# Kernel optimization log

Measured on AMD Instinct MI355X. Metric: run time of the kernel, lower is better.

The kernel has to match this reference:

```python
import jax, jax.numpy as jnp
import numpy as np

L, H, E, FF, MAXP, NKNOW = 4, 8, 512, 2048, 10, 1000
B, S = 4, 128
HD = E // H


def _layer_norm(x, g, b, eps=1e-5):
    m = x.mean(-1, keepdims=True)
    v = ((x - m) ** 2).mean(-1, keepdims=True)
    return (x - m) / jnp.sqrt(v + eps) * g + b


def setup_inputs() -> dict:
    key = jax.random.key(0)
    ks = jax.random.split(key, 16)
    x = jax.random.normal(ks[0], (B, S, E), jnp.float32)
    adj = jax.random.randint(ks[1], (B, S, S), 0, 2, jnp.int32)
    s_mask = jax.random.randint(ks[2], (B, S, S), 0, 2, jnp.int32)
    o_mask = jax.random.randint(ks[3], (B, S, S), 0, 2, jnp.int32)
    knowledge = jax.random.normal(ks[4], (NKNOW, E), jnp.float32)
    know_adj = jax.random.randint(ks[5], (B, S, S), 0, NKNOW, jnp.int64)
    pos_mask = jax.random.randint(ks[6], (S, S), 0, MAXP + 1, jnp.int32)
    # relative position embedding tables (padding_idx=0 -> row 0 zero)
    pe_k = jax.random.normal(ks[7], (MAXP + 1, HD), jnp.float32).at[0].set(0.0)
    pe_v = jax.random.normal(ks[8], (MAXP + 1, HD), jnp.float32).at[0].set(0.0)
    sc = 0.02
    # stacked per-layer parameters
    Wq = jax.random.normal(ks[9], (L, E, E), jnp.float32) * sc
    Wk = jax.random.normal(ks[10], (L, E, E), jnp.float32) * sc
    Wvs = jax.random.normal(ks[11], (L, E, E), jnp.float32) * sc
    Wvo = jax.random.normal(ks[12], (L, E, E), jnp.float32) * sc
    Wo = jax.random.normal(ks[13], (L, E, E), jnp.float32) * sc
    Wkn = jax.random.normal(ks[14], (L, E, E), jnp.float32) * sc
    kf = jax.random.split(ks[15], 4)
    w1 = jax.random.normal(kf[0], (L, FF, E), jnp.float32) * sc
    b1 = jnp.zeros((L, FF), jnp.float32)
    w2 = jax.random.normal(kf[1], (L, E, FF), jnp.float32) * sc
    b2 = jnp.zeros((L, E), jnp.float32)
    ln1_g = jnp.ones((L, E), jnp.float32)
    ln1_b = jnp.zeros((L, E), jnp.float32)
    ln2_g = jnp.ones((L, E), jnp.float32)
    ln2_b = jnp.zeros((L, E), jnp.float32)
    return dict(x=x, adj=adj, s_mask=s_mask, o_mask=o_mask, knowledge=knowledge,
                know_adj=know_adj, pos_mask=pos_mask, pe_k=pe_k, pe_v=pe_v,
                Wq=Wq, Wk=Wk, Wvs=Wvs, Wvo=Wvo, Wo=Wo, Wkn=Wkn,
                ln1_g=ln1_g, ln1_b=ln1_b, w1=w1, b1=b1, w2=w2, b2=b2,
                ln2_g=ln2_g, ln2_b=ln2_b)


def reference(x, adj, s_mask, o_mask, knowledge, know_adj, pos_mask, pe_k, pe_v,
              Wq, Wk, Wvs, Wvo, Wo, Wkn, ln1_g, ln1_b, w1, b1, w2, b2,
              ln2_g, ln2_b):
    bsz, slen, emb = x.shape
    hd = emb // H
    scaling = float(hd) ** (-0.5)
    # relative position embeddings, shared across batch/heads: [S,S,hd]
    pos = jnp.clip(pos_mask, 0, MAXP)
    rel_k = pe_k[pos]
    rel_v = pe_v[pos]
    adj_f = adj.astype(x.dtype)[:, None, :, :]          # [B,1,S,S]
    sm = s_mask.astype(x.dtype)[:, None, :, :, None]    # [B,1,S,S,1]
    om = o_mask.astype(x.dtype)[:, None, :, :, None]
    know_feat = knowledge[know_adj]                      # [B,S,S,E]

    def split_heads(t):  # [B,S,E] -> [B,H,S,hd]
        return t.reshape(bsz, slen, H, hd).transpose(0, 2, 1, 3)

    h = x
    for i in range(L):
        q = split_heads(h @ Wq[i].T)
        k = split_heads(h @ Wk[i].T)
        vs = split_heads(h @ Wvs[i].T)
        vo = split_heads(h @ Wvo[i].T)
        # knowledge projection -> [B,H,S,S,hd]
        know = (know_feat @ Wkn[i].T).reshape(bsz, slen, slen, H, hd).transpose(0, 3, 1, 2, 4)
        # multiplicative attention: q_i * (k_j + know_ij + rel_ij) summed over hd
        rel = (know + rel_k[None, None]) + k[:, :, None, :, :]
        scores = jnp.einsum('bhid,bhijd->bhij', q, rel) * scaling
        scores = scores - (1.0 - adj_f) * 1e30          # mask_logic
        attn = jax.nn.softmax(scores, axis=-1)           # [B,H,S,S]
        value = vs[:, :, None, :, :] * sm + vo[:, :, None, :, :] * om  # [B,H,S,S,hd]
        attn_sum = jnp.einsum('bhijd,bhij->bhid', value + rel_v[None, None], attn)
        out = attn_sum.transpose(0, 2, 1, 3).reshape(bsz, slen, emb) @ Wo[i].T
        h = _layer_norm(h + out, ln1_g[i], ln1_b[i])
        ff = jax.nn.relu(h @ w1[i].T + b1[i]) @ w2[i].T + b2[i]
        h = _layer_norm(h + ff, ln2_g[i], ln2_b[i])
    return h
```

## Files before the change

### kernel.cpp

```cpp
#include <hip/hip_runtime.h>

#define EE 512
#define SS 128
#define BB 4
#define NH 8
#define HD 64
#define FFD 2048
#define NL 4
#define LDQ 2048
#define KEXT 320
#define PSTR 136

typedef short bf16x8 __attribute__((ext_vector_type(8)));
typedef float f32x4 __attribute__((ext_vector_type(4)));

__device__ __forceinline__ ushort f2bf(float f) {
    uint u = __float_as_uint(f);
    return (ushort)((u + 0x7fffu + ((u >> 16) & 1u)) >> 16);
}
__device__ __forceinline__ float bflo(uint u) { return __uint_as_float(u << 16); }
__device__ __forceinline__ float bfhi(uint u) { return __uint_as_float(u & 0xffff0000u); }

__device__ __forceinline__ void gll16(const ushort* g, ushort* l) {
    __builtin_amdgcn_global_load_lds(
        (const __attribute__((address_space(1))) void*)g,
        (__attribute__((address_space(3))) void*)l, 16, 0, 0);
}

struct GemmJob {
    const ushort* A; const ushort* B;
    float* Cf; ushort* Cb; ushort* vext;
    const float* bias; const float* resid;
    int M, N, K, flags, nbx, base;
};

__global__ __launch_bounds__(256) void gemm_bf16(GemmJob j0, GemmJob j1, int njobs)
{
    __shared__ ushort As[4][2048];
    __shared__ ushort Bs[4][4096];
    GemmJob j = (njobs > 1 && (int)blockIdx.x >= j1.base) ? j1 : j0;
    const int bid = (int)blockIdx.x - j.base;
    const int by = bid / j.nbx, bx = bid % j.nbx;
    const int rowBase = by * 32, colBase = bx * 64;
    const int t = threadIdx.x, lane = t & 63, wid = t >> 6;
    const int wc = wid;
    const int Kd = j.K, Md = j.M, Nd = j.N;

    const ushort* Bg = j.B + (size_t)(colBase + lane) * Kd;
    int gr = rowBase + (lane & 31); if (gr >= Md) gr = Md - 1;
    const ushort* Ag = j.A + (size_t)gr * Kd + (2 * wid + (lane >> 5)) * 8;

    f32x4 acc[2];
#pragma unroll
    for (int m = 0; m < 2; ++m)
#pragma unroll
        for (int r = 0; r < 4; ++r) acc[m][r] = 0.f;

    auto STAGE = [&](int bf, int tt) {
        const int k0 = tt << 6;
        gll16(Bg + k0 + (2 * wid) * 8,     &Bs[bf][(2 * wid) * 512]);
        gll16(Bg + k0 + (2 * wid + 1) * 8, &Bs[bf][(2 * wid + 1) * 512]);
        gll16(Ag + k0,                     &As[bf][(2 * wid) * 256]);
    };
    auto COMPUTE = [&](int bf) {
#pragma unroll
        for (int kc = 0; kc < 2; ++kc) {
            const int c16 = kc * 4 + (lane >> 4);
            bf16x8 af[2], bfg;
#pragma unroll
            for (int m = 0; m < 2; ++m) {
                const int row = m * 16 + (lane & 15);
                af[m] = *(const bf16x8*)&As[bf][c16 * 256 + row * 8];
            }
            {
                const int rowb = wc * 16 + (lane & 15);
                bfg = *(const bf16x8*)&Bs[bf][c16 * 512 + rowb * 8];
            }
#pragma unroll
            for (int m = 0; m < 2; ++m)
                acc[m] = __builtin_amdgcn_mfma_f32_16x16x32_bf16(af[m], bfg, acc[m], 0, 0, 0);
        }
    };

    const int nt = Kd >> 6;
    STAGE(0, 0); STAGE(1, 1); STAGE(2, 2);
    asm volatile("s_waitcnt vmcnt(6)" ::: "memory");
    __builtin_amdgcn_s_barrier();
    for (int tt = 0; tt < nt; ++tt) {
        if (tt + 3 < nt) STAGE((tt + 3) & 3, tt + 3);
        COMPUTE(tt & 3);
        if (tt < nt - 1) {
            if (tt + 3 < nt)      asm volatile("s_waitcnt vmcnt(6)" ::: "memory");
            else if (tt + 2 < nt) asm volatile("s_waitcnt vmcnt(3)" ::: "memory");
            else                  asm volatile("s_waitcnt vmcnt(0)" ::: "memory");
            __builtin_amdgcn_s_barrier();
        }
    }

    const int cl = lane & 15, rh = lane >> 4;
#pragma unroll
    for (int m = 0; m < 2; ++m) {
        const int col = colBase + wc * 16 + cl;
#pragma unroll
        for (int r = 0; r < 4; ++r) {
            const int rr = rowBase + m * 16 + rh * 4 + r;
            if (rr < Md) {
                float v = acc[m][r];
                if (j.flags & 1) v += j.bias[col];
                if (j.flags & 2) v = fmaxf(v, 0.f);
                if (j.resid) v += j.resid[(size_t)rr * Nd + col];
                if ((j.flags & 4) && col >= 1024) {
                    const int cc = col - 1024;
                    const int hh = (cc >> 6) & 7, d = cc & 63, vv = cc >> 9;
                    const int bb = rr >> 7, jj2 = rr & 127;
                    j.vext[((size_t)((bb * 8 + hh) * 64 + d)) * KEXT + vv * 128 + jj2] = f2bf(v);
                } else {
                    if (j.Cf) j.Cf[(size_t)rr * Nd + col] = v;
                    if (j.Cb) j.Cb[(size_t)rr * Nd + col] = f2bf(v);
                }
            }
        }
    }
}

__global__ __launch_bounds__(256) void score_gemm(
    const ushort* __restrict__ qkvv, const ushort* __restrict__ kprojl,
    float* __restrict__ qk, float* __restrict__ qkk)
{
    __shared__ ushort As[2048];
    __shared__ ushort Bs[4096];
    const int t = threadIdx.x, lane = t & 63, wid = t >> 6;
    const int bid = blockIdx.x;
    const ushort *Abase, *Bbase;
    float* Cbase; int crs, rowBase, colBase;
    if (bid < 256) {
        const int q = bid >> 3, sub = bid & 7;
        const int b = q >> 3, h = q & 7;
        rowBase = (sub >> 1) * 32; colBase = (sub & 1) * 64;
        Abase = qkvv + (size_t)(b * SS) * LDQ + h * HD;
        Bbase = qkvv + (size_t)(b * SS) * LDQ + 512 + h * HD;
        Cbase = qk + (size_t)b * 131072 + h * 128;
        crs = 1024;
    } else {
        const int idx = bid - 256;
        const int h = idx >> 8, sub = idx & 255;
        rowBase = (sub >> 4) * 32; colBase = (sub & 15) * 64;
        Abase = qkvv + h * HD;
        Bbase = kprojl + h * HD;
        Cbase = qkk + (size_t)h * 1024;
        crs = 8192;
    }
    {
        const ushort* Bg = Bbase + (size_t)(colBase + lane) * LDQ;
        const ushort* Ag = Abase + (size_t)(rowBase + (lane & 31)) * LDQ
                           + (2 * wid + (lane >> 5)) * 8;
        gll16(Bg + (2 * wid) * 8,     &Bs[(2 * wid) * 512]);
        gll16(Bg + (2 * wid + 1) * 8, &Bs[(2 * wid + 1) * 512]);
        gll16(Ag,                     &As[(2 * wid) * 256]);
        asm volatile("s_waitcnt vmcnt(0)" ::: "memory");
        __builtin_amdgcn_s_barrier();
    }
    f32x4 acc[2];
#pragma unroll
    for (int m = 0; m < 2; ++m)
#pragma unroll
        for (int r = 0; r < 4; ++r) acc[m][r] = 0.f;
#pragma unroll
    for (int kc = 0; kc < 2; ++kc) {
        const int c16 = kc * 4 + (lane >> 4);
        bf16x8 af[2], bfg;
#pragma unroll
        for (int m = 0; m < 2; ++m) {
            const int row = m * 16 + (lane & 15);
            af[m] = *(const bf16x8*)&As[c16 * 256 + row * 8];
        }
        {
            const int rowb = wid * 16 + (lane & 15);
            bfg = *(const bf16x8*)&Bs[c16 * 512 + rowb * 8];
        }
#pragma unroll
        for (int m = 0; m < 2; ++m)
            acc[m] = __builtin_amdgcn_mfma_f32_16x16x32_bf16(af[m], bfg, acc[m], 0, 0, 0);
    }
    const int cl = lane & 15, rh = lane >> 4;
#pragma unroll
    for (int m = 0; m < 2; ++m) {
        const int col = colBase + wid * 16 + cl;
        const int row0 = rowBase + m * 16 + rh * 4;
#pragma unroll
        for (int r = 0; r < 4; ++r)
            Cbase[(size_t)(row0 + r) * crs + col] = acc[m][r];
    }
}

__global__ __launch_bounds__(256) void pv_kernel(
    const ushort* __restrict__ vext, const float* __restrict__ qk,
    const float* __restrict__ qkk,
    const int* __restrict__ know_adj, const int* __restrict__ pos_mask,
    const int* __restrict__ adj, const int* __restrict__ s_mask,
    const int* __restrict__ o_mask, ushort* __restrict__ asum)
{
    __shared__ ushort Ps[40 * PSTR];
    __shared__ ushort Bs[40 * 512];
    __shared__ float ap[16][11];
    const int blk = blockIdx.x;
    const int ib = blk & 7, h = (blk >> 3) & 7, b = blk >> 6;
    const int t = threadIdx.x, lane = t & 63, wid = t >> 6;

    if (t < 176) ap[t / 11][t % 11] = 0.f;
    __syncthreads();

    {
        const ushort* vbase = vext + ((size_t)((b * 8 + h) * 64) + lane) * KEXT;
#pragma unroll
        for (int s = 0; s < 5; ++s) {
            const int c = s * 8 + wid * 2;
            gll16(vbase + c * 8,       &Bs[c * 512]);
            gll16(vbase + (c + 1) * 8, &Bs[(c + 1) * 512]);
        }
    }

    {
        const int r = t >> 4, g = t & 15;
        const int i = ib * 16 + r;
        const int tok = b * 128 + i;
        const float* qkrow  = qk + (size_t)b * 131072 + (size_t)i * 1024 + h * 128 + g * 8;
        const float* qkkrow = qkk + (size_t)tok * 8192 + h * 1024;
        const int base = tok * 128 + g * 8;
        const int pb   = i * 128 + g * 8;
        int4 kn0 = *(const int4*)(know_adj + base), kn1 = *(const int4*)(know_adj + base + 4);
        int4 ad0 = *(const int4*)(adj + base),      ad1 = *(const int4*)(adj + base + 4);
        int4 sm0 = *(const int4*)(s_mask + base),   sm1 = *(const int4*)(s_mask + base + 4);
        int4 om0 = *(const int4*)(o_mask + base),   om1 = *(const int4*)(o_mask + base + 4);
        int4 po0 = *(const int4*)(pos_mask + pb),   po1 = *(const int4*)(pos_mask + pb + 4);
        float4 q0 = *(const float4*)qkrow,          q1 = *(const float4*)(qkrow + 4);
        int kn[8] = {kn0.x, kn0.y, kn0.z, kn0.w, kn1.x, kn1.y, kn1.z, kn1.w};
        int ad[8] = {ad0.x, ad0.y, ad0.z, ad0.w, ad1.x, ad1.y, ad1.z, ad1.w};
        int sm[8] = {sm0.x, sm0.y, sm0.z, sm0.w, sm1.x, sm1.y, sm1.z, sm1.w};
        int om[8] = {om0.x, om0.y, om0.z, om0.w, om1.x, om1.y, om1.z, om1.w};
        int po[8] = {po0.x, po0.y, po0.z, po0.w, po1.x, po1.y, po1.z, po1.w};
        float qv[8] = {q0.x, q0.y, q0.z, q0.w, q1.x, q1.y, q1.z, q1.w};
        float e[8];
        int pcl[8];
        float mx = -3e38f;
#pragma unroll
        for (int u = 0; u < 8; ++u) {
            int p = po[u]; p = p < 0 ? 0 : (p > 10 ? 10 : p);
            pcl[u] = p;
            float sc = (qv[u] + qkkrow[kn[u]] + qkkrow[1000 + p]) * 0.125f;
            if (!ad[u]) sc -= 1e30f;
            e[u] = sc; mx = fmaxf(mx, sc);
        }
        mx = fmaxf(mx, __shfl_xor(mx, 1));
        mx = fmaxf(mx, __shfl_xor(mx, 2));
        mx = fmaxf(mx, __shfl_xor(mx, 4));
        mx = fmaxf(mx, __shfl_xor(mx, 8));
        float sum = 0.f;
#pragma unroll
        for (int u = 0; u < 8; ++u) { e[u] = __expf(e[u] - mx); sum += e[u]; }
        sum += __shfl_xor(sum, 1);
        sum += __shfl_xor(sum, 2);
        sum += __shfl_xor(sum, 4);
        sum += __shfl_xor(sum, 8);
        const float inv = 1.f / sum;
        ushort p1v[8], p2v[8];
#pragma unroll
        for (int u = 0; u < 8; ++u) {
            const float a = e[u] * inv;
            p1v[u] = f2bf(a * (float)sm[u]);
            p2v[u] = f2bf(a * (float)om[u]);
            atomicAdd(&ap[r][pcl[u]], a);
        }
        *(uint4*)&Ps[g * PSTR + r * 8]        = *(uint4*)p1v;
        *(uint4*)&Ps[(16 + g) * PSTR + r * 8] = *(uint4*)p2v;
    }
    __syncthreads();

#pragma unroll
    for (int u = 0; u < 4; ++u) {
        const int idx = t * 4 + u;
        const int k = 256 + (idx & 63), rr = idx >> 6;
        const float v = (k < 267) ? ap[rr][k - 256] : 0.f;
        Ps[(k >> 3) * PSTR + rr * 8 + (k & 7)] = f2bf(v);
    }
    __syncthreads();

    f32x4 acc;
#pragma unroll
    for (int r = 0; r < 4; ++r) acc[r] = 0.f;
#pragma unroll
    for (int s = 0; s < 5; ++s) {
#pragma unroll
        for (int kc = 0; kc < 2; ++kc) {
            const int ch = s * 8 + kc * 4 + (lane >> 4);
            bf16x8 af = *(const bf16x8*)&Ps[ch * PSTR + (lane & 15) * 8];
            bf16x8 bfg = *(const bf16x8*)&Bs[ch * 512 + (wid * 16 + (lane & 15)) * 8];
            acc = __builtin_amdgcn_mfma_f32_16x16x32_bf16(af, bfg, acc, 0, 0, 0);
        }
    }
    const int cl = lane & 15, rh = lane >> 4;
    const int col = wid * 16 + cl;
#pragma unroll
    for (int r = 0; r < 4; ++r) {
        const int rowv = rh * 4 + r;
        asum[(size_t)(b * 128 + ib * 16 + rowv) * 512 + h * 64 + col] = f2bf(acc[r]);
    }
}

struct PrepArgs {
    const float *Wq, *Wk, *Wvs, *Wvo, *Wo, *Wkn, *w1, *w2, *know, *x, *pek, *pev;
    ushort *wqkvv, *wo, *wkn, *w1b, *w2b, *knowb, *hb, *kpe, *vext;
    float *h;
};
#define P4_WQKVV 1048576
#define P4_B1 (P4_WQKVV + 262144)
#define P4_B2 (P4_B1 + 262144)
#define P4_B3 (P4_B2 + 1048576)
#define P4_B4 (P4_B3 + 1048576)
#define P4_B5 (P4_B4 + 128000)
#define P4_B6 (P4_B5 + 65536)
#define P4_B7 (P4_B6 + 5632)
#define P4_TOT (P4_B7 + 32768)

__global__ __launch_bounds__(256) void prep_kernel(PrepArgs pa)
{
    const int i = blockIdx.x * 256 + threadIdx.x;
    if (i >= P4_TOT) return;
    if (i >= P4_B7) {
        const int k = i - P4_B7;
        const int bh = k >> 10, r2 = k & 1023, d = r2 >> 4, s4 = r2 & 15;
        ushort o[4];
#pragma unroll
        for (int c = 0; c < 4; ++c) {
            const int p = s4 * 4 + c;
            o[c] = (p < 11) ? f2bf(pa.pev[p * 64 + d]) : (ushort)0;
        }
        *(ushort4*)(pa.vext + ((size_t)(bh * 64 + d)) * KEXT + 256 + s4 * 4)
            = *(ushort4*)o;
        return;
    }
    const float4* src;
    ushort4* dst;
    if (i < P4_WQKVV) {
        const int l = i >> 18, r = i & 262143, q = r >> 16;
        const float* s = (q == 0 ? pa.Wq : q == 1 ? pa.Wk : q == 2 ? pa.Wvs : pa.Wvo);
        src = (const float4*)s + l * 65536 + (r & 65535);
        dst = (ushort4*)pa.wqkvv + i;
    } else if (i < P4_B1) {
        const int k = i - P4_WQKVV;
        src = (const float4*)pa.Wo + k; dst = (ushort4*)pa.wo + k;
    } else if (i < P4_B2) {
        const int k = i - P4_B1;
        src = (const float4*)pa.Wkn + k; dst = (ushort4*)pa.wkn + k;
    } else if (i < P4_B3) {
        const int k = i - P4_B2;
        src = (const float4*)pa.w1 + k; dst = (ushort4*)pa.w1b + k;
    } else if (i < P4_B4) {
        const int k = i - P4_B3;
        src = (const float4*)pa.w2 + k; dst = (ushort4*)pa.w2b + k;
    } else if (i < P4_B5) {
        const int k = i - P4_B4;
        src = (const float4*)pa.know + k; dst = (ushort4*)pa.knowb + k;
    } else if (i < P4_B6) {
        const int k = i - P4_B5;
        src = (const float4*)pa.x + k; dst = (ushort4*)pa.hb + k;
        ((float4*)pa.h)[k] = *src;
    } else {
        const int k = i - P4_B6;
        const int c4 = k * 4;
        const int p = c4 >> 11, col = c4 & 2047, d = col & 63;
        src = (const float4*)(pa.pek + p * 64 + d);
        dst = (ushort4*)(pa.kpe + (size_t)(1000 + p) * 2048 + col);
    }
    float4 v = *src;
    ushort4 o; o.x = f2bf(v.x); o.y = f2bf(v.y); o.z = f2bf(v.z); o.w = f2bf(v.w);
    *dst = o;
}

__global__ __launch_bounds__(256) void ln_kernel(
    const float* __restrict__ X, const float* __restrict__ g,
    const float* __restrict__ bt, float* __restrict__ Yf,
    ushort* __restrict__ Yb, int rows)
{
    const int w = threadIdx.x >> 6, lane = threadIdx.x & 63;
    const int row = blockIdx.x * 4 + w;
    if (row >= rows) return;
    const float* x = X + (size_t)row * EE;
    float4 v0 = ((const float4*)x)[lane];
    float4 v1 = ((const float4*)x)[lane + 64];
    float s  = v0.x + v0.y + v0.z + v0.w + v1.x + v1.y + v1.z + v1.w;
    float q2 = v0.x*v0.x + v0.y*v0.y + v0.z*v0.z + v0.w*v0.w
             + v1.x*v1.x + v1.y*v1.y + v1.z*v1.z + v1.w*v1.w;
#pragma unroll
    for (int o = 32; o; o >>= 1) { s += __shfl_xor(s, o); q2 += __shfl_xor(q2, o); }
    const float mean = s * (1.f / EE);
    const float var  = q2 * (1.f / EE) - mean * mean;
    const float rstd = rsqrtf(var + 1e-5f);
    float4 g0 = ((const float4*)g)[lane],  g1 = ((const float4*)g)[lane + 64];
    float4 b0 = ((const float4*)bt)[lane], b1 = ((const float4*)bt)[lane + 64];
    float4 o0, o1;
    o0.x = (v0.x - mean) * rstd * g0.x + b0.x;
    o0.y = (v0.y - mean) * rstd * g0.y + b0.y;
    o0.z = (v0.z - mean) * rstd * g0.z + b0.z;
    o0.w = (v0.w - mean) * rstd * g0.w + b0.w;
    o1.x = (v1.x - mean) * rstd * g1.x + b1.x;
    o1.y = (v1.y - mean) * rstd * g1.y + b1.y;
    o1.z = (v1.z - mean) * rstd * g1.z + b1.z;
    o1.w = (v1.w - mean) * rstd * g1.w + b1.w;
    float* y = Yf + (size_t)row * EE;
    ((float4*)y)[lane] = o0;
    ((float4*)y)[lane + 64] = o1;
    ushort* yb = Yb + (size_t)row * EE;
    ushort4 p0, p1;
    p0.x = f2bf(o0.x); p0.y = f2bf(o0.y); p0.z = f2bf(o0.z); p0.w = f2bf(o0.w);
    p1.x = f2bf(o1.x); p1.y = f2bf(o1.y); p1.z = f2bf(o1.z); p1.w = f2bf(o1.w);
    ((ushort4*)yb)[lane] = p0;
    ((ushort4*)yb)[lane + 64] = p1;
}

extern "C" void kernel_launch(void* const* d_in, const int* in_sizes, int n_in,
                              void* d_out, int out_size, void* d_ws, size_t ws_size,
                              hipStream_t stream)
{
    const float* x         = (const float*)d_in[0];
    const int*   adj       = (const int*)d_in[1];
    const int*   s_mask    = (const int*)d_in[2];
    const int*   o_mask    = (const int*)d_in[3];
    const float* knowledge = (const float*)d_in[4];
    const int*   know_adj  = (const int*)d_in[5];
    const int*   pos_mask  = (const int*)d_in[6];
    const float* pe_k      = (const float*)d_in[7];
    const float* pe_v      = (const float*)d_in[8];
    const float* Wq        = (const float*)d_in[9];
    const float* Wk        = (const float*)d_in[10];
    const float* Wvs       = (const float*)d_in[11];
    const float* Wvo       = (const float*)d_in[12];
    const float* Wo        = (const float*)d_in[13];
    const float* Wkn       = (const float*)d_in[14];
    const float* ln1_g     = (const float*)d_in[15];
    const float* ln1_b     = (const float*)d_in[16];
    const float* w1        = (const float*)d_in[17];
    const float* b1        = (const float*)d_in[18];
    const float* w2        = (const float*)d_in[19];
    const float* b2        = (const float*)d_in[20];
    const float* ln2_g     = (const float*)d_in[21];
    const float* ln2_b     = (const float*)d_in[22];

    const int NTOK = BB * SS;
    const size_t NTE = (size_t)NTOK * EE;

    float*  h      = (float*)d_ws;
    float*  xt     = h + NTE;
    float*  qk     = xt + NTE;
    float*  qkk    = qk + (size_t)NTOK * 1024;
    ushort* hb     = (ushort*)(qkk + (size_t)NTOK * 8192);
    ushort* qkvv   = hb + NTE;
    ushort* kprojb = qkvv + (size_t)NTOK * LDQ;
    ushort* asumb  = kprojb + (size_t)1024 * LDQ;
    ushort* ffnb   = asumb + NTE;
    ushort* wqkvv  = ffnb + (size_t)NTOK * FFD;
    ushort* wob    = wqkvv + (size_t)NL * 4 * EE * EE;
    ushort* wknb   = wob + (size_t)NL * EE * EE;
    ushort* w1b    = wknb + (size_t)NL * EE * EE;
    ushort* w2b    = w1b + (size_t)NL * FFD * EE;
    ushort* knowb  = w2b + (size_t)NL * EE * FFD;
    ushort* vextb  = knowb + (size_t)1000 * EE;

    PrepArgs pa;
    pa.Wq = Wq; pa.Wk = Wk; pa.Wvs = Wvs; pa.Wvo = Wvo; pa.Wo = Wo; pa.Wkn = Wkn;
    pa.w1 = w1; pa.w2 = w2; pa.know = knowledge; pa.x = x; pa.pek = pe_k; pa.pev = pe_v;
    pa.wqkvv = wqkvv; pa.wo = wob; pa.wkn = wknb; pa.w1b = w1b; pa.w2b = w2b;
    pa.knowb = knowb; pa.hb = hb; pa.h = h; pa.kpe = kprojb; pa.vext = vextb;
    prep_kernel<<<dim3((P4_TOT + 255) / 256), dim3(256), 0, stream>>>(pa);

    const dim3 blk(256);
    for (int l = 0; l < NL; ++l) {
        GemmJob jq{};
        jq.A = hb; jq.B = wqkvv + (size_t)l * 4 * EE * EE;
        jq.Cb = qkvv; jq.vext = vextb; jq.flags = 4;
        jq.M = NTOK; jq.N = 4 * EE; jq.K = EE;
        jq.nbx = 32; jq.base = 0;
        if (l == 0) {
            GemmJob jk{};
            jk.A = knowb; jk.B = wknb;
            jk.Cb = kprojb; jk.M = 1000; jk.N = NL * EE; jk.K = EE;
            jk.nbx = 32; jk.base = 512;
            gemm_bf16<<<dim3(512 + 1024), blk, 0, stream>>>(jq, jk, 2);
        } else {
            gemm_bf16<<<dim3(512), blk, 0, stream>>>(jq, jq, 1);
        }

        score_gemm<<<dim3(2304), blk, 0, stream>>>(qkvv, kprojb + (size_t)l * EE,
                                                   qk, qkk);

        pv_kernel<<<dim3(256), blk, 0, stream>>>(vextb, qk, qkk, know_adj, pos_mask,
                                                 adj, s_mask, o_mask, asumb);

        GemmJob jo{};
        jo.A = asumb; jo.B = wob + (size_t)l * EE * EE;
        jo.Cf = xt; jo.resid = h; jo.M = NTOK; jo.N = EE; jo.K = EE;
        jo.nbx = 8; jo.base = 0;
        gemm_bf16<<<dim3(128), blk, 0, stream>>>(jo, jo, 1);

        ln_kernel<<<dim3(128), blk, 0, stream>>>(xt, ln1_g + l * EE, ln1_b + l * EE,
                                                 h, hb, NTOK);

        GemmJob jf1{};
        jf1.A = hb; jf1.B = w1b + (size_t)l * FFD * EE;
        jf1.Cb = ffnb; jf1.bias = b1 + (size_t)l * FFD; jf1.flags = 3;
        jf1.M = NTOK; jf1.N = FFD; jf1.K = EE; jf1.nbx = 32; jf1.base = 0;
        gemm_bf16<<<dim3(512), blk, 0, stream>>>(jf1, jf1, 1);

        GemmJob jf2{};
        jf2.A = ffnb; jf2.B = w2b + (size_t)l * EE * FFD;
        jf2.Cf = xt; jf2.bias = b2 + (size_t)l * EE; jf2.resid = h; jf2.flags = 1;
        jf2.M = NTOK; jf2.N = EE; jf2.K = FFD; jf2.nbx = 8; jf2.base = 0;
        gemm_bf16<<<dim3(128), blk, 0, stream>>>(jf2, jf2, 1);

        float* lnout = (l == NL - 1) ? (float*)d_out : h;
        ln_kernel<<<dim3(128), blk, 0, stream>>>(xt, ln2_g + l * EE, ln2_b + l * EE,
                                                 lnout, hb, NTOK);
    }
}
```

Measured before the change: 503.8 us.

## Enlarge GEMM tiles to 64x64 with 2x2 warp layout and triple buffering

The bf16 GEMM and score GEMM kernels move from 32x64 to 64x64 output tiles. Each wave now computes a 32x32 sub-tile (2x2 MFMAs) instead of 32x16, which raises operand reuse from LDS. The GEMM pipeline goes from 4-stage to 3-stage buffering to fit the larger A tiles, and all grid sizes are halved to match. The trade-off is fewer blocks: the smaller GEMMs (Wo and FFN2, now 64 blocks) leave most of the MI355X's CUs idle, and the shallower prefetch hides less load latency.

Result: slower. 536.2 us (+6.4%).

```diff
diff --git a/kernel.cpp b/kernel.cpp
--- a/kernel.cpp
+++ b/kernel.cpp
@@ -36,87 +36,97 @@
 
 __global__ __launch_bounds__(256) void gemm_bf16(GemmJob j0, GemmJob j1, int njobs)
 {
-    __shared__ ushort As[4][2048];
-    __shared__ ushort Bs[4][4096];
+    __shared__ ushort As[3][4096];
+    __shared__ ushort Bs[3][4096];
     GemmJob j = (njobs > 1 && (int)blockIdx.x >= j1.base) ? j1 : j0;
     const int bid = (int)blockIdx.x - j.base;
     const int by = bid / j.nbx, bx = bid % j.nbx;
-    const int rowBase = by * 32, colBase = bx * 64;
+    const int rowBase = by * 64, colBase = bx * 64;
     const int t = threadIdx.x, lane = t & 63, wid = t >> 6;
-    const int wc = wid;
+    const int wr = wid >> 1, wc = wid & 1;
     const int Kd = j.K, Md = j.M, Nd = j.N;
 
+    int gr = rowBase + lane; if (gr >= Md) gr = Md - 1;
+    const ushort* Ag = j.A + (size_t)gr * Kd;
     const ushort* Bg = j.B + (size_t)(colBase + lane) * Kd;
-    int gr = rowBase + (lane & 31); if (gr >= Md) gr = Md - 1;
-    const ushort* Ag = j.A + (size_t)gr * Kd + (2 * wid + (lane >> 5)) * 8;
-
-    f32x4 acc[2];
+
+    f32x4 acc[2][2];
 #pragma unroll
     for (int m = 0; m < 2; ++m)
 #pragma unroll
-        for (int r = 0; r < 4; ++r) acc[m][r] = 0.f;
+        for (int n = 0; n < 2; ++n)
+#pragma unroll
+            for (int r = 0; r < 4; ++r) acc[m][n][r] = 0.f;
 
     auto STAGE = [&](int bf, int tt) {
         const int k0 = tt << 6;
+        gll16(Ag + k0 + (2 * wid) * 8,     &As[bf][(2 * wid) * 512]);
+        gll16(Ag + k0 + (2 * wid + 1) * 8, &As[bf][(2 * wid + 1) * 512]);
         gll16(Bg + k0 + (2 * wid) * 8,     &Bs[bf][(2 * wid) * 512]);
         gll16(Bg + k0 + (2 * wid + 1) * 8, &Bs[bf][(2 * wid + 1) * 512]);
-        gll16(Ag + k0,                     &As[bf][(2 * wid) * 256]);
     };
     auto COMPUTE = [&](int bf) {
 #pragma unroll
         for (int kc = 0; kc < 2; ++kc) {
             const int c16 = kc * 4 + (lane >> 4);
-            bf16x8 af[2], bfg;
-#pragma unroll
-            for (int m = 0; m < 2; ++m) {
-                const int row = m * 16 + (lane & 15);
-                af[m] = *(const bf16x8*)&As[bf][c16 * 256 + row * 8];
-            }
-            {
-                const int rowb = wc * 16 + (lane & 15);
-                bfg = *(const bf16x8*)&Bs[bf][c16 * 512 + rowb * 8];
-            }
+            bf16x8 af[2], bfr[2];
 #pragma unroll
             for (int m = 0; m < 2; ++m)
-                acc[m] = __builtin_amdgcn_mfma_f32_16x16x32_bf16(af[m], bfg, acc[m], 0, 0, 0);
+                af[m] = *(const bf16x8*)&As[bf][c16 * 512 + (wr * 32 + m * 16 + (lane & 15)) * 8];
+#pragma unroll
+            for (int n = 0; n < 2; ++n)
+                bfr[n] = *(const bf16x8*)&Bs[bf][c16 * 512 + (wc * 32 + n * 16 + (lane & 15)) * 8];
+#pragma unroll
+            for (int m = 0; m < 2; ++m)
+#pragma unroll
+                for (int n = 0; n < 2; ++n)
+                    acc[m][n] = __builtin_amdgcn_mfma_f32_16x16x32_bf16(
+                        af[m], bfr[n], acc[m][n], 0, 0, 0);
         }
     };
 
     const int nt = Kd >> 6;
-    STAGE(0, 0); STAGE(1, 1); STAGE(2, 2);
-    asm volatile("s_waitcnt vmcnt(6)" ::: "memory");
+    STAGE(0, 0);
+    STAGE(1, 1);
+    asm volatile("s_waitcnt vmcnt(4)" ::: "memory");
     __builtin_amdgcn_s_barrier();
+    int bc = 0, bs = 2;
     for (int tt = 0; tt < nt; ++tt) {
-        if (tt + 3 < nt) STAGE((tt + 3) & 3, tt + 3);
-        COMPUTE(tt & 3);
+        const bool more = (tt + 2) < nt;
+        if (more) STAGE(bs, tt + 2);
+        COMPUTE(bc);
         if (tt < nt - 1) {
-            if (tt + 3 < nt)      asm volatile("s_waitcnt vmcnt(6)" ::: "memory");
-            else if (tt + 2 < nt) asm volatile("s_waitcnt vmcnt(3)" ::: "memory");
-            else                  asm volatile("s_waitcnt vmcnt(0)" ::: "memory");
+            if (more) asm volatile("s_waitcnt vmcnt(4)" ::: "memory");
+            else      asm volatile("s_waitcnt vmcnt(0)" ::: "memory");
             __builtin_amdgcn_s_barrier();
         }
+        bc = bc == 2 ? 0 : bc + 1;
+        bs = bs == 2 ? 0 : bs + 1;
     }
 
     const int cl = lane & 15, rh = lane >> 4;
 #pragma unroll
     for (int m = 0; m < 2; ++m) {
-        const int col = colBase + wc * 16 + cl;
-#pragma unroll
-        for (int r = 0; r < 4; ++r) {
-            const int rr = rowBase + m * 16 + rh * 4 + r;
-            if (rr < Md) {
-                float v = acc[m][r];
-                if (j.flags & 1) v += j.bias[col];
-                if (j.flags & 2) v = fmaxf(v, 0.f);
-                if (j.resid) v += j.resid[(size_t)rr * Nd + col];
-                if ((j.flags & 4) && col >= 1024) {
-                    const int cc = col - 1024;
-                    const int hh = (cc >> 6) & 7, d = cc & 63, vv = cc >> 9;
-                    const int bb = rr >> 7, jj2 = rr & 127;
-                    j.vext[((size_t)((bb * 8 + hh) * 64 + d)) * KEXT + vv * 128 + jj2] = f2bf(v);
-                } else {
-                    if (j.Cf) j.Cf[(size_t)rr * Nd + col] = v;
-                    if (j.Cb) j.Cb[(size_t)rr * Nd + col] = f2bf(v);
+#pragma unroll
+        for (int n = 0; n < 2; ++n) {
+            const int col = colBase + wc * 32 + n * 16 + cl;
+#pragma unroll
+            for (int r = 0; r < 4; ++r) {
+                const int rr = rowBase + wr * 32 + m * 16 + rh * 4 + r;
+                if (rr < Md) {
+                    float v = acc[m][n][r];
+                    if (j.flags & 1) v += j.bias[col];
+                    if (j.flags & 2) v = fmaxf(v, 0.f);
+                    if (j.resid) v += j.resid[(size_t)rr * Nd + col];
+                    if ((j.flags & 4) && col >= 1024) {
+                        const int cc = col - 1024;
+                        const int hh = (cc >> 6) & 7, d = cc & 63, vv = cc >> 9;
+                        const int bb = rr >> 7, jj2 = rr & 127;
+                        j.vext[((size_t)((bb * 8 + hh) * 64 + d)) * KEXT + vv * 128 + jj2] = f2bf(v);
+                    } else {
+                        if (j.Cf) j.Cf[(size_t)rr * Nd + col] = v;
+                        if (j.Cb) j.Cb[(size_t)rr * Nd + col] = f2bf(v);
+                    }
                 }
             }
         }
@@ -127,69 +137,75 @@
     const ushort* __restrict__ qkvv, const ushort* __restrict__ kprojl,
     float* __restrict__ qk, float* __restrict__ qkk)
 {
-    __shared__ ushort As[2048];
+    __shared__ ushort As[4096];
     __shared__ ushort Bs[4096];
     const int t = threadIdx.x, lane = t & 63, wid = t >> 6;
+    const int wr = wid >> 1, wc = wid & 1;
     const int bid = blockIdx.x;
     const ushort *Abase, *Bbase;
     float* Cbase; int crs, rowBase, colBase;
-    if (bid < 256) {
-        const int q = bid >> 3, sub = bid & 7;
+    if (bid < 128) {
+        const int q = bid >> 2, sub = bid & 3;
         const int b = q >> 3, h = q & 7;
-        rowBase = (sub >> 1) * 32; colBase = (sub & 1) * 64;
+        rowBase = (sub >> 1) * 64; colBase = (sub & 1) * 64;
         Abase = qkvv + (size_t)(b * SS) * LDQ + h * HD;
         Bbase = qkvv + (size_t)(b * SS) * LDQ + 512 + h * HD;
         Cbase = qk + (size_t)b * 131072 + h * 128;
         crs = 1024;
     } else {
-        const int idx = bid - 256;
-        const int h = idx >> 8, sub = idx & 255;
-        rowBase = (sub >> 4) * 32; colBase = (sub & 15) * 64;
+        const int idx = bid - 128;
+        const int h = idx >> 7, sub = idx & 127;
+        rowBase = (sub >> 4) * 64; colBase = (sub & 15) * 64;
         Abase = qkvv + h * HD;
         Bbase = kprojl + h * HD;
         Cbase = qkk + (size_t)h * 1024;
         crs = 8192;
     }
     {
+        const ushort* Ag = Abase + (size_t)(rowBase + lane) * LDQ;
         const ushort* Bg = Bbase + (size_t)(colBase + lane) * LDQ;
-        const ushort* Ag = Abase + (size_t)(rowBase + (lane & 31)) * LDQ
-                           + (2 * wid + (lane >> 5)) * 8;
+        gll16(Ag + (2 * wid) * 8,     &As[(2 * wid) * 512]);
+        gll16(Ag + (2 * wid + 1) * 8, &As[(2 * wid + 1) * 512]);
         gll16(Bg + (2 * wid) * 8,     &Bs[(2 * wid) * 512]);
         gll16(Bg + (2 * wid + 1) * 8, &Bs[(2 * wid + 1) * 512]);
-        gll16(Ag,                     &As[(2 * wid) * 256]);
         asm volatile("s_waitcnt vmcnt(0)" ::: "memory");
         __builtin_amdgcn_s_barrier();
     }
-    f32x4 acc[2];
+    f32x4 acc[2][2];
 #pragma unroll
     for (int m = 0; m < 2; ++m)
 #pragma unroll
-        for (int r = 0; r < 4; ++r) acc[m][r] = 0.f;
+        for (int n = 0; n < 2; ++n)
+#pragma unroll
+            for (int r = 0; r < 4; ++r) acc[m][n][r] = 0.f;
 #pragma unroll
     for (int kc = 0; kc < 2; ++kc) {
         const int c16 = kc * 4 + (lane >> 4);
-        bf16x8 af[2], bfg;
-#pragma unroll
-        for (int m = 0; m < 2; ++m) {
-            const int row = m * 16 + (lane & 15);
-            af[m] = *(const bf16x8*)&As[c16 * 256 + row * 8];
-        }
-        {
-            const int rowb = wid * 16 + (lane & 15);
-            bfg = *(const bf16x8*)&Bs[c16 * 512 + rowb * 8];
-        }
+        bf16x8 af[2], bfr[2];
 #pragma unroll
         for (int m = 0; m < 2; ++m)
-            acc[m] = __builtin_amdgcn_mfma_f32_16x16x32_bf16(af[m], bfg, acc[m], 0, 0, 0);
+            af[m] = *(const bf16x8*)&As[c16 * 512 + (wr * 32 + m * 16 + (lane & 15)) * 8];
+#pragma unroll
+        for (int n = 0; n < 2; ++n)
+            bfr[n] = *(const bf16x8*)&Bs[c16 * 512 + (wc * 32 + n * 16 + (lane & 15)) * 8];
+#pragma unroll
+        for (int m = 0; m < 2; ++m)
+#pragma unroll
+            for (int n = 0; n < 2; ++n)
+                acc[m][n] = __builtin_amdgcn_mfma_f32_16x16x32_bf16(
+                    af[m], bfr[n], acc[m][n], 0, 0, 0);
     }
     const int cl = lane & 15, rh = lane >> 4;
 #pragma unroll
     for (int m = 0; m < 2; ++m) {
-        const int col = colBase + wid * 16 + cl;
-        const int row0 = rowBase + m * 16 + rh * 4;
-#pragma unroll
-        for (int r = 0; r < 4; ++r)
-            Cbase[(size_t)(row0 + r) * crs + col] = acc[m][r];
+#pragma unroll
+        for (int n = 0; n < 2; ++n) {
+            const int col = colBase + wc * 32 + n * 16 + cl;
+            const int row0 = rowBase + wr * 32 + m * 16 + rh * 4;
+#pragma unroll
+            for (int r = 0; r < 4; ++r)
+                Cbase[(size_t)(row0 + r) * crs + col] = acc[m][n][r];
+        }
     }
 }
 
@@ -484,13 +500,13 @@
             GemmJob jk{};
             jk.A = knowb; jk.B = wknb;
             jk.Cb = kprojb; jk.M = 1000; jk.N = NL * EE; jk.K = EE;
-            jk.nbx = 32; jk.base = 512;
-            gemm_bf16<<<dim3(512 + 1024), blk, 0, stream>>>(jq, jk, 2);
+            jk.nbx = 32; jk.base = 256;
+            gemm_bf16<<<dim3(256 + 512), blk, 0, stream>>>(jq, jk, 2);
         } else {
-            gemm_bf16<<<dim3(512), blk, 0, stream>>>(jq, jq, 1);
-        }
-
-        score_gemm<<<dim3(2304), blk, 0, stream>>>(qkvv, kprojb + (size_t)l * EE,
+            gemm_bf16<<<dim3(256), blk, 0, stream>>>(jq, jq, 1);
+        }
+
+        score_gemm<<<dim3(1152), blk, 0, stream>>>(qkvv, kprojb + (size_t)l * EE,
                                                    qk, qkk);
 
         pv_kernel<<<dim3(256), blk, 0, stream>>>(vextb, qk, qkk, know_adj, pos_mask,
@@ -500,7 +516,7 @@
         jo.A = asumb; jo.B = wob + (size_t)l * EE * EE;
         jo.Cf = xt; jo.resid = h; jo.M = NTOK; jo.N = EE; jo.K = EE;
         jo.nbx = 8; jo.base = 0;
-        gemm_bf16<<<dim3(128), blk, 0, stream>>>(jo, jo, 1);
+        gemm_bf16<<<dim3(64), blk, 0, stream>>>(jo, jo, 1);
 
         ln_kernel<<<dim3(128), blk, 0, stream>>>(xt, ln1_g + l * EE, ln1_b + l * EE,
                                                  h, hb, NTOK);
@@ -509,13 +525,13 @@
         jf1.A = hb; jf1.B = w1b + (size_t)l * FFD * EE;
         jf1.Cb = ffnb; jf1.bias = b1 + (size_t)l * FFD; jf1.flags = 3;
         jf1.M = NTOK; jf1.N = FFD; jf1.K = EE; jf1.nbx = 32; jf1.base = 0;
-        gemm_bf16<<<dim3(512), blk, 0, stream>>>(jf1, jf1, 1);
+        gemm_bf16<<<dim3(256), blk, 0, stream>>>(jf1, jf1, 1);
 
         GemmJob jf2{};
         jf2.A = ffnb; jf2.B = w2b + (size_t)l * EE * FFD;
         jf2.Cf = xt; jf2.bias = b2 + (size_t)l * EE; jf2.resid = h; jf2.flags = 1;
         jf2.M = NTOK; jf2.N = EE; jf2.K = FFD; jf2.nbx = 8; jf2.base = 0;
-        gemm_bf16<<<dim3(128), blk, 0, stream>>>(jf2, jf2, 1);
+        gemm_bf16<<<dim3(64), blk, 0, stream>>>(jf2, jf2, 1);
 
         float* lnout = (l == NL - 1) ? (float*)d_out : h;
         ln_kernel<<<dim3(128), blk, 0, stream>>>(xt, ln2_g + l * EE, ln2_b + l * EE,
```
